# Kernel optimization log

Measured on AMD Instinct MI355X. Metric: run time of the kernel, lower is better.

The kernel has to match this reference:

```python
import jax, jax.numpy as jnp
import numpy as np

HEAD_SIZE = 64

def setup_inputs() -> dict:
    key = jax.random.key(0)
    ks = jax.random.split(key, 6)
    B, T, D, H, HS = 4, 2048, 1024, 16, HEAD_SIZE
    s = 1.0 / np.sqrt(D)
    return {
        "x": jax.random.normal(ks[0], (B, T, D), jnp.float32),
        "Wq": jax.random.normal(ks[1], (H, D, HS), jnp.float32) * s,
        "Wk": jax.random.normal(ks[2], (H, D, HS), jnp.float32) * s,
        "Wv": jax.random.normal(ks[3], (H, D, HS), jnp.float32) * s,
        "Wp": jax.random.normal(ks[4], (D, D), jnp.float32) * s,
        "bp": jnp.zeros((D,), jnp.float32),
    }

def reference(x, Wq, Wk, Wv, Wp, bp):
    B, T, D = x.shape
    H, _, HS = Wq.shape
    # per-head projections (bias-free Linears), stacked over heads
    q = jnp.einsum('btd,hde->bhte', x, Wq)
    k = jnp.einsum('btd,hde->bhte', x, Wk)
    v = jnp.einsum('btd,hde->bhte', x, Wv)
    scores = jnp.einsum('bhqe,bhke->bhqk', q, k) / jnp.sqrt(jnp.float32(HS))
    causal = jnp.tril(jnp.ones((T, T), bool))  # mask[:T,:T]
    scores = jnp.where(causal, scores, -jnp.inf)
    w = jax.nn.softmax(scores, axis=-1)  # dropout p=0.0 -> identity
    out = jnp.einsum('bhqk,bhke->bhqe', w, v)
    # concat heads along last dim: [B,T,H*HS] == [B,T,D]
    out = out.transpose(0, 2, 1, 3).reshape(B, T, H * HS)
    return out @ Wp.T + bp  # note: Wp stored as [out,in] like nn.Linear
```

## Files before the change

kernel.cpp:

```cpp
#include <hip/hip_runtime.h>
#include <hip/hip_bf16.h>

typedef unsigned short u16;
typedef unsigned int u32;
typedef __attribute__((ext_vector_type(8))) short short8;
typedef __attribute__((ext_vector_type(4))) float f32x4;

#define B_ 4
#define T_ 2048
#define D_ 1024
#define H_ 16
#define HS_ 64
#define BT (B_*T_)

__device__ __forceinline__ float bf2f(u16 b){ union{u32 u; float f;} v; v.u=((u32)b)<<16; return v.f; }
__device__ __forceinline__ u16 f2bf(float f){
    __hip_bfloat16 h = __float2bfloat16(f);
    union{__hip_bfloat16 h; u16 u;} v; v.h = h; return v.u;
}
__device__ __forceinline__ void split2(float x, u16& h, u16& l){
    u16 hb = f2bf(x);
    float fh = bf2f(hb);
    h = hb; l = f2bf(x - fh);
}
union U4 { u16 s[4]; uint2 v; };
union S8 { u16 s[8]; short8 v; };

#define GLD16(g,l) __builtin_amdgcn_global_load_lds( \
    (__attribute__((address_space(1))) void*)(u16*)(g), \
    (__attribute__((address_space(3))) void*)(l), 16, 0, 0)

__device__ __forceinline__ int swz(int row, int col){
    return row*64 + (((col>>3) ^ (row&7))<<3) + (col&7);
}
#define FCHK(r) (((r)>>1)&3)

#define DPPMV(x, ctrl) __int_as_float(__builtin_amdgcn_update_dpp(0, __float_as_int(x), (ctrl), 0xF, 0xF, true))

__global__ __launch_bounds__(256) void split_f32(const float* __restrict__ src,
                                                 u16* __restrict__ dh, u16* __restrict__ dl,
                                                 int n8)
{
    int i = blockIdx.x*256 + threadIdx.x;
    const int stride = gridDim.x*256;
    for (; i < n8; i += stride){
        float4 a = *(const float4*)(src + (size_t)i*8);
        float4 b = *(const float4*)(src + (size_t)i*8 + 4);
        S8 hh, ll;
        split2(a.x, hh.s[0], ll.s[0]); split2(a.y, hh.s[1], ll.s[1]);
        split2(a.z, hh.s[2], ll.s[2]); split2(a.w, hh.s[3], ll.s[3]);
        split2(b.x, hh.s[4], ll.s[4]); split2(b.y, hh.s[5], ll.s[5]);
        split2(b.z, hh.s[6], ll.s[6]); split2(b.w, hh.s[7], ll.s[7]);
        *(short8*)(dh + (size_t)i*8) = hh.v;
        *(short8*)(dl + (size_t)i*8) = ll.v;
    }
}

__global__ __launch_bounds__(256) void pack_w(const float* __restrict__ Wq,
                                              const float* __restrict__ Wk,
                                              const float* __restrict__ Wv,
                                              u16* __restrict__ Wth,
                                              u16* __restrict__ Wtl)
{
    __shared__ float Tl[64*68];
    const int h = blockIdx.x, dt = blockIdx.y, z = blockIdx.z;
    const float* src = (z==0) ? Wq : ((z==1) ? Wk : Wv);
    const int t = threadIdx.x;
    const int d0 = dt*64;
    #pragma unroll
    for (int i=0;i<4;++i){
        int ci = t + 256*i;
        int dr = ci>>4, ec = ci&15;
        float4 v = *(const float4*)(src + ((size_t)h*D_ + d0+dr)*HS_ + ec*4);
        *(float4*)(Tl + dr*68 + ec*4) = v;
    }
    __syncthreads();
    #pragma unroll
    for (int i=0;i<4;++i){
        int ci = t + 256*i;
        int e = ci>>4, dc = ci&15;
        U4 hh, ll;
        #pragma unroll
        for (int j=0;j<4;++j){
            float f = Tl[(dc*4+j)*68 + e];
            split2(f, hh.s[j], ll.s[j]);
        }
        int n = z*D_ + h*HS_ + e;
        *(uint2*)(Wth + (size_t)n*D_ + d0 + dc*4) = hh.v;
        *(uint2*)(Wtl + (size_t)n*D_ + d0 + dc*4) = ll.v;
    }
}

template<bool PS>
__global__ __launch_bounds__(256) void gemm_qkv(const float* __restrict__ x,
                                                const u16* __restrict__ xh, const u16* __restrict__ xl,
                                                const u16* __restrict__ Wth,
                                                const u16* __restrict__ Wtl,
                                                float* __restrict__ qo,
                                                u16* __restrict__ qho, u16* __restrict__ qlo,
                                                u16* __restrict__ kho, u16* __restrict__ klo,
                                                u16* __restrict__ vth, u16* __restrict__ vtl)
{
    __shared__ u16 Ash[128*32], Asl[128*32];
    __shared__ u16 Bsh[128*32], Bsl[128*32];
    const int n0 = blockIdx.x*128, m0 = blockIdx.y*128;
    const int t = threadIdx.x;
    const int w = t>>6, lane = t&63, quad = lane>>4, l16 = lane&15;
    const int wm = (w>>1)*64, wn = (w&1)*64;
    f32x4 acc[4][4];
    #pragma unroll
    for (int i=0;i<4;++i)
        #pragma unroll
        for (int j=0;j<4;++j) acc[i][j] = (f32x4){0.f,0.f,0.f,0.f};
    for (int kt=0; kt<32; ++kt){
        const int k0 = kt*32;
        #pragma unroll
        for (int i=0;i<2;++i){
            int ci = t + 256*i;
            int row = ci>>2, c = ci&3;
            int cs = c ^ FCHK(row);
            GLD16(Wth + (size_t)(n0+row)*D_ + k0 + cs*8, Bsh + ci*8);
            GLD16(Wtl + (size_t)(n0+row)*D_ + k0 + cs*8, Bsl + ci*8);
        }
        if constexpr(PS){
            #pragma unroll
            for (int i=0;i<2;++i){
                int ci = t + 256*i;
                int row = ci>>2, c = ci&3;
                int cs = c ^ FCHK(row);
                GLD16(xh + (size_t)(m0+row)*D_ + k0 + cs*8, Ash + ci*8);
                GLD16(xl + (size_t)(m0+row)*D_ + k0 + cs*8, Asl + ci*8);
            }
        } else {
            #pragma unroll
            for (int i=0;i<4;++i){
                int ci = t + 256*i;
                int row = ci>>3, c4 = ci&7;
                float4 av = *(const float4*)(x + (size_t)(m0+row)*D_ + k0 + c4*4);
                U4 hh, ll;
                split2(av.x, hh.s[0], ll.s[0]); split2(av.y, hh.s[1], ll.s[1]);
                split2(av.z, hh.s[2], ll.s[2]); split2(av.w, hh.s[3], ll.s[3]);
                int off = row*32 + ((((c4>>1) ^ FCHK(row))<<3) | ((c4&1)<<2));
                *(uint2*)(Ash + off) = hh.v;
                *(uint2*)(Asl + off) = ll.v;
            }
        }
        __syncthreads();
        short8 afh[4], afl[4], bfh[4], bfl[4];
        #pragma unroll
        for (int mi=0;mi<4;++mi){
            const int rr = wm+mi*16+l16;
            const int off = rr*32 + ((quad ^ FCHK(rr))<<3);
            afh[mi] = *(const short8*)(Ash + off);
            afl[mi] = *(const short8*)(Asl + off);
        }
        #pragma unroll
        for (int ni=0;ni<4;++ni){
            const int rr = wn+ni*16+l16;
            const int off = rr*32 + ((quad ^ FCHK(rr))<<3);
            bfh[ni] = *(const short8*)(Bsh + off);
            bfl[ni] = *(const short8*)(Bsl + off);
        }
        #pragma unroll
        for (int mi=0;mi<4;++mi)
            #pragma unroll
            for (int ni=0;ni<4;++ni){
                acc[mi][ni] = __builtin_amdgcn_mfma_f32_16x16x32_bf16(afh[mi], bfh[ni], acc[mi][ni], 0,0,0);
                acc[mi][ni] = __builtin_amdgcn_mfma_f32_16x16x32_bf16(afh[mi], bfl[ni], acc[mi][ni], 0,0,0);
                acc[mi][ni] = __builtin_amdgcn_mfma_f32_16x16x32_bf16(afl[mi], bfh[ni], acc[mi][ni], 0,0,0);
            }
        __syncthreads();
    }
    const int z = n0 >> 10;
    if (z <= 1){
        if constexpr(PS){
            u16* dh = z ? kho : qho;
            u16* dl = z ? klo : qlo;
            #pragma unroll
            for (int ni=0;ni<4;++ni){
                const int nloc = (n0 & 1023) + wn + ni*16 + l16;
                #pragma unroll
                for (int mi=0;mi<4;++mi){
                    const int row = m0 + wm + mi*16 + quad*4;
                    #pragma unroll
                    for (int r=0;r<4;++r){
                        u16 hh, ll; split2(acc[mi][ni][r], hh, ll);
                        dh[(size_t)(row+r)*D_ + nloc] = hh;
                        dl[(size_t)(row+r)*D_ + nloc] = ll;
                    }
                }
            }
        } else {
            if (z == 0){
                #pragma unroll
                for (int ni=0;ni<4;++ni){
                    const int nloc = (n0 & 1023) + wn + ni*16 + l16;
                    #pragma unroll
                    for (int mi=0;mi<4;++mi){
                        const int row = m0 + wm + mi*16 + quad*4;
                        #pragma unroll
                        for (int r=0;r<4;++r)
                            qo[(size_t)(row+r)*D_ + nloc] = acc[mi][ni][r];
                    }
                }
            } else {
                #pragma unroll
                for (int ni=0;ni<4;++ni){
                    const int nloc = (n0 & 1023) + wn + ni*16 + l16;
                    #pragma unroll
                    for (int mi=0;mi<4;++mi){
                        const int row = m0 + wm + mi*16 + quad*4;
                        #pragma unroll
                        for (int r=0;r<4;++r){
                            u16 hh, ll; split2(acc[mi][ni][r], hh, ll);
                            kho[(size_t)(row+r)*D_ + nloc] = hh;
                            klo[(size_t)(row+r)*D_ + nloc] = ll;
                        }
                    }
                }
            }
        }
    } else {
        #pragma unroll
        for (int ni=0;ni<4;++ni){
            const int nloc = (n0 & 1023) + wn + ni*16 + l16;
            const int hloc = nloc>>6, e = nloc&63;
            #pragma unroll
            for (int mi=0;mi<4;++mi){
                const int rowb = m0 + wm + mi*16 + quad*4;
                const int bidx = rowb >> 11, tloc = rowb & 2047;
                U4 hh, ll;
                #pragma unroll
                for (int r=0;r<4;++r) split2(acc[mi][ni][r], hh.s[r], ll.s[r]);
                const size_t adr = ((size_t)((bidx*16 + hloc)*64 + e))*T_ + tloc;
                *(uint2*)(vth + adr) = hh.v;
                *(uint2*)(vtl + adr) = ll.v;
            }
        }
    }
}

template<bool PS>
__global__ __launch_bounds__(512, 2) void attn(const float* __restrict__ qf,
                                            const u16* __restrict__ qh, const u16* __restrict__ ql,
                                            const u16* __restrict__ kh, const u16* __restrict__ kl,
                                            const u16* __restrict__ vth, const u16* __restrict__ vtl,
                                            float* __restrict__ att,
                                            u16* __restrict__ atth, u16* __restrict__ attl)
{
    __shared__ u16 Ksh[64*64], Ksl[64*64];
    __shared__ u16 Vsh[64*64], Vsl[64*64];
    __shared__ u16 Pb[8*32*64];
    const int x = blockIdx.y & 7;
    const int bh = (blockIdx.x << 3) | (blockIdx.y >> 3);
    const int b = bh >> 4, h = bh & 15;
    const int t = threadIdx.x;
    const int w = t>>6, lane = t&63, quad = lane>>4, l16 = lane&15;

    u16* Pm = Pb + w*2048;

    const int srow = t>>3, sc = t&7;
    const int slo = swz(srow, sc*8);
    uint4 pkh, pkl, pvh, pvl;
    {
        const size_t gk = ((size_t)(b*T_ + srow))*D_ + h*64 + sc*8;
        pkh = *(const uint4*)(kh + gk);
        pkl = *(const uint4*)(kl + gk);
        const size_t gv = ((size_t)(bh*64 + srow))*T_ + sc*8;
        pvh = *(const uint4*)(vth + gv);
        pvl = *(const uint4*)(vtl + gv);
    }

    #pragma unroll 1
    for (int seg=0; seg<2; ++seg){
        const int qi = seg ? x : (15 - x);
        const int qrow = qi*128 + w*16;

        short8 qh_[2], ql_[2];
        if constexpr(PS){
            const size_t qb = ((size_t)(b*T_ + qrow + l16))*D_ + h*64;
            #pragma unroll
            for (int ks=0;ks<2;++ks){
                qh_[ks] = *(const short8*)(qh + qb + ks*32 + quad*8);
                ql_[ks] = *(const short8*)(ql + qb + ks*32 + quad*8);
            }
        } else {
            const float* qp = qf + ((size_t)(b*T_ + qrow + l16))*D_ + h*64;
            #pragma unroll
            for (int ks=0;ks<2;++ks){
                float4 a0 = *(const float4*)(qp + ks*32 + quad*8);
                float4 a1 = *(const float4*)(qp + ks*32 + quad*8 + 4);
                S8 hh, ll;
                split2(a0.x, hh.s[0], ll.s[0]); split2(a0.y, hh.s[1], ll.s[1]);
                split2(a0.z, hh.s[2], ll.s[2]); split2(a0.w, hh.s[3], ll.s[3]);
                split2(a1.x, hh.s[4], ll.s[4]); split2(a1.y, hh.s[5], ll.s[5]);
                split2(a1.z, hh.s[6], ll.s[6]); split2(a1.w, hh.s[7], ll.s[7]);
                qh_[ks] = hh.v; ql_[ks] = ll.v;
            }
        }
        f32x4 o[4];
        #pragma unroll
        for (int i=0;i<4;++i) o[i] = (f32x4){0.f,0.f,0.f,0.f};
        float m_i[4], l_i[4];
        #pragma unroll
        for (int r=0;r<4;++r){ m_i[r] = -INFINITY; l_i[r] = 0.f; }

        const int kvT = 2*qi + 2;
        for (int kvt=0; kvt<kvT; ++kvt){
            __syncthreads();
            *(uint4*)(Ksh + slo) = pkh;
            *(uint4*)(Ksl + slo) = pkl;
            *(uint4*)(Vsh + slo) = pvh;
            *(uint4*)(Vsl + slo) = pvl;
            __syncthreads();

            const int nk = (kvt+1 < kvT) ? (kvt+1) : ((seg==0) ? 0 : -1);
            if (nk >= 0){
                const size_t gk = ((size_t)(b*T_ + nk*64 + srow))*D_ + h*64 + sc*8;
                pkh = *(const uint4*)(kh + gk);
                pkl = *(const uint4*)(kl + gk);
                const size_t gv = ((size_t)(bh*64 + srow))*T_ + nk*64 + sc*8;
                pvh = *(const uint4*)(vth + gv);
                pvl = *(const uint4*)(vtl + gv);
            }

            float s[4][4];
            __builtin_amdgcn_s_setprio(1);
            #pragma unroll
            for (int ni=0;ni<4;++ni){
                f32x4 sa = (f32x4){0.f,0.f,0.f,0.f};
                const int row = ni*16 + l16;
                #pragma unroll
                for (int ks=0;ks<2;++ks){
                    const int co = swz(row, ks*32 + quad*8);
                    short8 k8h = *(const short8*)(Ksh + co);
                    short8 k8l = *(const short8*)(Ksl + co);
                    sa = __builtin_amdgcn_mfma_f32_16x16x32_bf16(qh_[ks], k8h, sa, 0,0,0);
                    sa = __builtin_amdgcn_mfma_f32_16x16x32_bf16(qh_[ks], k8l, sa, 0,0,0);
                    sa = __builtin_amdgcn_mfma_f32_16x16x32_bf16(ql_[ks], k8h, sa, 0,0,0);
                }
                #pragma unroll
                for (int r=0;r<4;++r) s[ni][r] = sa[r]*0.125f;
            }
            __builtin_amdgcn_s_setprio(0);
            if (kvt*64 + 63 > qrow){
                #pragma unroll
                for (int ni=0;ni<4;++ni){
                    const int colabs = kvt*64 + ni*16 + l16;
                    #pragma unroll
                    for (int r=0;r<4;++r){
                        const int rowabs = qrow + quad*4 + r;
                        if (colabs > rowabs) s[ni][r] = -INFINITY;
                    }
                }
            }
            float alpha[4];
            #pragma unroll
            for (int r=0;r<4;++r){
                float rm = fmaxf(fmaxf(s[0][r],s[1][r]), fmaxf(s[2][r],s[3][r]));
                rm = fmaxf(rm, DPPMV(rm, 0xB1));
                rm = fmaxf(rm, DPPMV(rm, 0x4E));
                rm = fmaxf(rm, DPPMV(rm, 0x124));
                rm = fmaxf(rm, DPPMV(rm, 0x128));
                const float mnew = fmaxf(m_i[r], rm);
                alpha[r] = __expf(m_i[r] - mnew);
                m_i[r] = mnew;
                #pragma unroll
                for (int ni=0;ni<4;++ni) s[ni][r] = __expf(s[ni][r] - mnew);
                float rs = s[0][r]+s[1][r]+s[2][r]+s[3][r];
                rs += DPPMV(rs, 0xB1);
                rs += DPPMV(rs, 0x4E);
                rs += DPPMV(rs, 0x124);
                rs += DPPMV(rs, 0x128);
                l_i[r] = l_i[r]*alpha[r] + rs;
            }
            #pragma unroll
            for (int ni=0;ni<4;++ni)
                #pragma unroll
                for (int r=0;r<4;++r) o[ni][r] *= alpha[r];

            u16 ph[4][4], pl[4][4];
            #pragma unroll
            for (int ni=0;ni<4;++ni)
                #pragma unroll
                for (int r=0;r<4;++r)
                    split2(s[ni][r], ph[ni][r], pl[ni][r]);
            #pragma unroll
            for (int ni=0;ni<4;++ni)
                #pragma unroll
                for (int r=0;r<4;++r){
                    Pm[swz(quad*4+r,      ni*16 + l16)] = ph[ni][r];
                    Pm[swz(16 + quad*4+r, ni*16 + l16)] = pl[ni][r];
                }
            __asm__ volatile("s_waitcnt lgkmcnt(0)" ::: "memory");
            short8 pah[2], pal[2];
            #pragma unroll
            for (int ks=0;ks<2;++ks){
                pah[ks] = *(const short8*)(Pm + swz(l16,      ks*32 + quad*8));
                pal[ks] = *(const short8*)(Pm + swz(16 + l16, ks*32 + quad*8));
            }

            __builtin_amdgcn_s_setprio(1);
            #pragma unroll
            for (int ni=0;ni<4;++ni){
                const int row = ni*16 + l16;
                #pragma unroll
                for (int ks=0;ks<2;++ks){
                    const int co = swz(row, ks*32 + quad*8);
                    short8 v8h = *(const short8*)(Vsh + co);
                    short8 v8l = *(const short8*)(Vsl + co);
                    o[ni] = __builtin_amdgcn_mfma_f32_16x16x32_bf16(pah[ks], v8h, o[ni], 0,0,0);
                    o[ni] = __builtin_amdgcn_mfma_f32_16x16x32_bf16(pah[ks], v8l, o[ni], 0,0,0);
                    o[ni] = __builtin_amdgcn_mfma_f32_16x16x32_bf16(pal[ks], v8h, o[ni], 0,0,0);
                }
            }
            __builtin_amdgcn_s_setprio(0);
        }
        const size_t ob = (size_t)(b*T_ + qrow);
        #pragma unroll
        for (int ni=0;ni<4;++ni){
            const int col = h*64 + ni*16 + l16;
            #pragma unroll
            for (int r=0;r<4;++r){
                const float v = o[ni][r] / l_i[r];
                const size_t idx = (ob + quad*4 + r)*D_ + col;
                if constexpr(PS){
                    u16 hh, ll; split2(v, hh, ll);
                    atth[idx] = hh; attl[idx] = ll;
                } else {
                    att[idx] = v;
                }
            }
        }
    }
}

template<bool PS>
__global__ __launch_bounds__(256) void gemm_bt(const float* __restrict__ A,
                                               const u16* __restrict__ Ath, const u16* __restrict__ Atl,
                                               const float* __restrict__ Bt,
                                               const u16* __restrict__ Bth, const u16* __restrict__ Btl,
                                               float* __restrict__ C,
                                               const float* __restrict__ bias,
                                               int M, int N, int K)
{
    __shared__ u16 Ash[128*32], Asl[128*32];
    __shared__ u16 Bsh[128*32], Bsl[128*32];
    const int n0 = blockIdx.x*128, m0 = blockIdx.y*128;
    const int t = threadIdx.x;
    const int w = t>>6, lane = t&63, quad = lane>>4, l16 = lane&15;
    const int wm = (w>>1)*64, wn = (w&1)*64;
    f32x4 acc[4][4];
    #pragma unroll
    for (int i=0;i<4;++i)
        #pragma unroll
        for (int j=0;j<4;++j) acc[i][j] = (f32x4){0.f,0.f,0.f,0.f};
    const int kT = K >> 5;
    for (int kt=0; kt<kT; ++kt){
        const int k0 = kt*32;
        if constexpr(PS){
            #pragma unroll
            for (int i=0;i<2;++i){
                int ci = t + 256*i;
                int row = ci>>2, c = ci&3;
                int cs = c ^ FCHK(row);
                GLD16(Ath + (size_t)(m0+row)*K + k0 + cs*8, Ash + ci*8);
                GLD16(Atl + (size_t)(m0+row)*K + k0 + cs*8, Asl + ci*8);
                GLD16(Bth + (size_t)(n0+row)*K + k0 + cs*8, Bsh + ci*8);
                GLD16(Btl + (size_t)(n0+row)*K + k0 + cs*8, Bsl + ci*8);
            }
        } else {
            #pragma unroll
            for (int i=0;i<4;++i){
                int ci = t + 256*i;
                int row = ci>>3, c4 = ci&7;
                float4 av = *(const float4*)(A  + (size_t)(m0+row)*K + k0 + c4*4);
                float4 bv = *(const float4*)(Bt + (size_t)(n0+row)*K + k0 + c4*4);
                U4 ah, al, bh, bl;
                split2(av.x, ah.s[0], al.s[0]); split2(av.y, ah.s[1], al.s[1]);
                split2(av.z, ah.s[2], al.s[2]); split2(av.w, ah.s[3], al.s[3]);
                split2(bv.x, bh.s[0], bl.s[0]); split2(bv.y, bh.s[1], bl.s[1]);
                split2(bv.z, bh.s[2], bl.s[2]); split2(bv.w, bh.s[3], bl.s[3]);
                int off = row*32 + ((((c4>>1) ^ FCHK(row))<<3) | ((c4&1)<<2));
                *(uint2*)(Ash + off) = ah.v;
                *(uint2*)(Asl + off) = al.v;
                *(uint2*)(Bsh + off) = bh.v;
                *(uint2*)(Bsl + off) = bl.v;
            }
        }
        __syncthreads();
        short8 afh[4], afl[4], bfh[4], bfl[4];
        #pragma unroll
        for (int mi=0;mi<4;++mi){
            const int rr = wm+mi*16+l16;
            const int off = rr*32 + ((quad ^ FCHK(rr))<<3);
            afh[mi] = *(const short8*)(Ash + off);
            afl[mi] = *(const short8*)(Asl + off);
        }
        #pragma unroll
        for (int ni=0;ni<4;++ni){
            const int rr = wn+ni*16+l16;
            const int off = rr*32 + ((quad ^ FCHK(rr))<<3);
            bfh[ni] = *(const short8*)(Bsh + off);
            bfl[ni] = *(const short8*)(Bsl + off);
        }
        #pragma unroll
        for (int mi=0;mi<4;++mi)
            #pragma unroll
            for (int ni=0;ni<4;++ni){
                acc[mi][ni] = __builtin_amdgcn_mfma_f32_16x16x32_bf16(afh[mi], bfh[ni], acc[mi][ni], 0,0,0);
                acc[mi][ni] = __builtin_amdgcn_mfma_f32_16x16x32_bf16(afh[mi], bfl[ni], acc[mi][ni], 0,0,0);
                acc[mi][ni] = __builtin_amdgcn_mfma_f32_16x16x32_bf16(afl[mi], bfh[ni], acc[mi][ni], 0,0,0);
            }
        __syncthreads();
    }
    #pragma unroll
    for (int ni=0;ni<4;++ni){
        const int col = n0 + wn + ni*16 + l16;
        const float bv = bias ? bias[col] : 0.f;
        #pragma unroll
        for (int mi=0;mi<4;++mi){
            const int row = m0 + wm + mi*16 + quad*4;
            #pragma unroll
            for (int r=0;r<4;++r)
                C[(size_t)(row+r)*N + col] = acc[mi][ni][r] + bv;
        }
    }
}

extern "C" void kernel_launch(void* const* d_in, const int* in_sizes, int n_in,
                              void* d_out, int out_size, void* d_ws, size_t ws_size,
                              hipStream_t stream)
{
    const float* x  = (const float*)d_in[0];
    const float* Wq = (const float*)d_in[1];
    const float* Wk = (const float*)d_in[2];
    const float* Wv = (const float*)d_in[3];
    const float* Wp = (const float*)d_in[4];
    const float* bp = (const float*)d_in[5];
    float* out = (float*)d_out;

    const size_t NE = (size_t)BT*D_;
    const size_t NEED = (10*NE + 2*(size_t)D_*D_)*2;

    if (ws_size >= NEED){
        u16* xh   = (u16*)d_ws;
        u16* xl   = xh + NE;
        u16* qh   = xl + NE;
        u16* ql   = qh + NE;
        u16* kh   = ql + NE;
        u16* kl   = kh + NE;
        u16* vth  = kl + NE;
        u16* vtl  = vth + NE;
        u16* atth = vtl + NE;
        u16* attl = atth + NE;
        u16* Wph  = attl + NE;
        u16* Wpl  = Wph + (size_t)D_*D_;
        u16* Wth  = atth;
        u16* Wtl  = Wth + (size_t)3072*D_;

        split_f32<<<1024, 256, 0, stream>>>(x,  xh,  xl,  (int)(NE/8));
        split_f32<<<512,  256, 0, stream>>>(Wp, Wph, Wpl, (int)(((size_t)D_*D_)/8));
        pack_w   <<<dim3(16,16,3), 256, 0, stream>>>(Wq, Wk, Wv, Wth, Wtl);
        gemm_qkv<true><<<dim3(24, BT/128), 256, 0, stream>>>(x, xh, xl, Wth, Wtl,
                                                             nullptr, qh, ql, kh, kl, vth, vtl);
        attn<true><<<dim3(T_/256, B_*H_), 512, 0, stream>>>(nullptr, qh, ql, kh, kl, vth, vtl,
                                                            nullptr, atth, attl);
        gemm_bt<true><<<dim3(8, BT/128), 256, 0, stream>>>(nullptr, atth, attl,
                                                           nullptr, Wph, Wpl,
                                                           out, bp, BT, D_, D_);
    } else {
        float* q   = (float*)d_ws;
        u16*  kh   = (u16*)(q + NE);
        u16*  kl   = kh + NE;
        u16*  vth  = kl + NE;
        u16*  vtl  = vth + NE;
        float* att = (float*)(vtl + NE);
        u16*  Wth  = (u16*)att;
        u16*  Wtl  = Wth + (size_t)3072*D_;

        pack_w   <<<dim3(16,16,3), 256, 0, stream>>>(Wq, Wk, Wv, Wth, Wtl);
        gemm_qkv<false><<<dim3(24, BT/128), 256, 0, stream>>>(x, nullptr, nullptr, Wth, Wtl,
                                                              q, nullptr, nullptr, kh, kl, vth, vtl);
        attn<false><<<dim3(T_/256, B_*H_), 512, 0, stream>>>(q, nullptr, nullptr, kh, kl, vth, vtl,
                                                             att, nullptr, nullptr);
        gemm_bt<false><<<dim3(8, BT/128), 256, 0, stream>>>(att, nullptr, nullptr,
                                                            Wp, nullptr, nullptr,
                                                            out, bp, BT, D_, D_);
    }
}
```

Baseline: 492.7 us.

## Shrink attention blocks to 4 waves with 64-row query tiles and halved P buffer

The attention kernel now runs 256-thread blocks, four waves covering 64 query rows, instead of 512-thread blocks covering 128 rows. The grid is remapped to 8x128 with paired causal tiles (31-px, px), and each thread loads two 16-byte chunks per K/V tile. The per-wave P staging buffer is halved by writing the high and low bf16 halves in sequence through the same space. The second barrier now comes after issuing the next tile's global loads. The aim is higher occupancy and finer load balance, at the cost of more K/V reloads per query row and an extra LDS round trip for P.

Result: slower. 659.3 us (+33.8%).

```diff
diff --git a/kernel.cpp b/kernel.cpp
--- a/kernel.cpp
+++ b/kernel.cpp
@@ -241,7 +241,7 @@
 }
 
 template<bool PS>
-__global__ __launch_bounds__(512, 2) void attn(const float* __restrict__ qf,
+__global__ __launch_bounds__(256, 4) void attn(const float* __restrict__ qf,
                                             const u16* __restrict__ qh, const u16* __restrict__ ql,
                                             const u16* __restrict__ kh, const u16* __restrict__ kl,
                                             const u16* __restrict__ vth, const u16* __restrict__ vtl,
@@ -250,31 +250,33 @@
 {
     __shared__ u16 Ksh[64*64], Ksl[64*64];
     __shared__ u16 Vsh[64*64], Vsl[64*64];
-    __shared__ u16 Pb[8*32*64];
-    const int x = blockIdx.y & 7;
-    const int bh = (blockIdx.x << 3) | (blockIdx.y >> 3);
+    __shared__ u16 Pb[4*16*64];
+    const int bx = blockIdx.x, by = blockIdx.y;
+    const int bh = ((by & 7) << 3) | bx;
+    const int px = by >> 3;
     const int b = bh >> 4, h = bh & 15;
     const int t = threadIdx.x;
     const int w = t>>6, lane = t&63, quad = lane>>4, l16 = lane&15;
 
-    u16* Pm = Pb + w*2048;
-
-    const int srow = t>>3, sc = t&7;
-    const int slo = swz(srow, sc*8);
-    uint4 pkh, pkl, pvh, pvl;
+    u16* Pm = Pb + w*1024;
+
+    const int srow = t>>2, sc = t&3;
+    const int slo0 = swz(srow, sc*8);
+    const int slo1 = swz(srow, sc*8 + 32);
+    uint4 pkh0, pkh1, pkl0, pkl1, pvh0, pvh1, pvl0, pvl1;
     {
         const size_t gk = ((size_t)(b*T_ + srow))*D_ + h*64 + sc*8;
-        pkh = *(const uint4*)(kh + gk);
-        pkl = *(const uint4*)(kl + gk);
+        pkh0 = *(const uint4*)(kh + gk);  pkh1 = *(const uint4*)(kh + gk + 32);
+        pkl0 = *(const uint4*)(kl + gk);  pkl1 = *(const uint4*)(kl + gk + 32);
         const size_t gv = ((size_t)(bh*64 + srow))*T_ + sc*8;
-        pvh = *(const uint4*)(vth + gv);
-        pvl = *(const uint4*)(vtl + gv);
+        pvh0 = *(const uint4*)(vth + gv); pvh1 = *(const uint4*)(vth + gv + 32);
+        pvl0 = *(const uint4*)(vtl + gv); pvl1 = *(const uint4*)(vtl + gv + 32);
     }
 
     #pragma unroll 1
     for (int seg=0; seg<2; ++seg){
-        const int qi = seg ? x : (15 - x);
-        const int qrow = qi*128 + w*16;
+        const int qi = seg ? px : (31 - px);
+        const int qrow = qi*64 + w*16;
 
         short8 qh_[2], ql_[2];
         if constexpr(PS){
@@ -305,24 +307,23 @@
         #pragma unroll
         for (int r=0;r<4;++r){ m_i[r] = -INFINITY; l_i[r] = 0.f; }
 
-        const int kvT = 2*qi + 2;
+        const int kvT = qi + 1;
         for (int kvt=0; kvt<kvT; ++kvt){
             __syncthreads();
-            *(uint4*)(Ksh + slo) = pkh;
-            *(uint4*)(Ksl + slo) = pkl;
-            *(uint4*)(Vsh + slo) = pvh;
-            *(uint4*)(Vsl + slo) = pvl;
-            __syncthreads();
-
+            *(uint4*)(Ksh + slo0) = pkh0;  *(uint4*)(Ksh + slo1) = pkh1;
+            *(uint4*)(Ksl + slo0) = pkl0;  *(uint4*)(Ksl + slo1) = pkl1;
+            *(uint4*)(Vsh + slo0) = pvh0;  *(uint4*)(Vsh + slo1) = pvh1;
+            *(uint4*)(Vsl + slo0) = pvl0;  *(uint4*)(Vsl + slo1) = pvl1;
             const int nk = (kvt+1 < kvT) ? (kvt+1) : ((seg==0) ? 0 : -1);
             if (nk >= 0){
                 const size_t gk = ((size_t)(b*T_ + nk*64 + srow))*D_ + h*64 + sc*8;
-                pkh = *(const uint4*)(kh + gk);
-                pkl = *(const uint4*)(kl + gk);
+                pkh0 = *(const uint4*)(kh + gk);  pkh1 = *(const uint4*)(kh + gk + 32);
+                pkl0 = *(const uint4*)(kl + gk);  pkl1 = *(const uint4*)(kl + gk + 32);
                 const size_t gv = ((size_t)(bh*64 + srow))*T_ + nk*64 + sc*8;
-                pvh = *(const uint4*)(vth + gv);
-                pvl = *(const uint4*)(vtl + gv);
-            }
+                pvh0 = *(const uint4*)(vth + gv); pvh1 = *(const uint4*)(vth + gv + 32);
+                pvl0 = *(const uint4*)(vtl + gv); pvl1 = *(const uint4*)(vtl + gv + 32);
+            }
+            __syncthreads();
 
             float s[4][4];
             __builtin_amdgcn_s_setprio(1);
@@ -388,17 +389,24 @@
             #pragma unroll
             for (int ni=0;ni<4;++ni)
                 #pragma unroll
-                for (int r=0;r<4;++r){
-                    Pm[swz(quad*4+r,      ni*16 + l16)] = ph[ni][r];
-                    Pm[swz(16 + quad*4+r, ni*16 + l16)] = pl[ni][r];
-                }
+                for (int r=0;r<4;++r)
+                    Pm[swz(quad*4+r, ni*16 + l16)] = ph[ni][r];
             __asm__ volatile("s_waitcnt lgkmcnt(0)" ::: "memory");
             short8 pah[2], pal[2];
             #pragma unroll
-            for (int ks=0;ks<2;++ks){
-                pah[ks] = *(const short8*)(Pm + swz(l16,      ks*32 + quad*8));
-                pal[ks] = *(const short8*)(Pm + swz(16 + l16, ks*32 + quad*8));
-            }
+            for (int ks=0;ks<2;++ks)
+                pah[ks] = *(const short8*)(Pm + swz(l16, ks*32 + quad*8));
+            __asm__ volatile("" ::: "memory");
+            #pragma unroll
+            for (int ni=0;ni<4;++ni)
+                #pragma unroll
+                for (int r=0;r<4;++r)
+                    Pm[swz(quad*4+r, ni*16 + l16)] = pl[ni][r];
+            __asm__ volatile("s_waitcnt lgkmcnt(0)" ::: "memory");
+            #pragma unroll
+            for (int ks=0;ks<2;++ks)
+                pal[ks] = *(const short8*)(Pm + swz(l16, ks*32 + quad*8));
+            __asm__ volatile("" ::: "memory");
 
             __builtin_amdgcn_s_setprio(1);
             #pragma unroll
@@ -564,8 +572,8 @@
         pack_w   <<<dim3(16,16,3), 256, 0, stream>>>(Wq, Wk, Wv, Wth, Wtl);
         gemm_qkv<true><<<dim3(24, BT/128), 256, 0, stream>>>(x, xh, xl, Wth, Wtl,
                                                              nullptr, qh, ql, kh, kl, vth, vtl);
-        attn<true><<<dim3(T_/256, B_*H_), 512, 0, stream>>>(nullptr, qh, ql, kh, kl, vth, vtl,
-                                                            nullptr, atth, attl);
+        attn<true><<<dim3(8, 128), 256, 0, stream>>>(nullptr, qh, ql, kh, kl, vth, vtl,
+                                                     nullptr, atth, attl);
         gemm_bt<true><<<dim3(8, BT/128), 256, 0, stream>>>(nullptr, atth, attl,
                                                            nullptr, Wph, Wpl,
                                                            out, bp, BT, D_, D_);
@@ -582,8 +590,8 @@
         pack_w   <<<dim3(16,16,3), 256, 0, stream>>>(Wq, Wk, Wv, Wth, Wtl);
         gemm_qkv<false><<<dim3(24, BT/128), 256, 0, stream>>>(x, nullptr, nullptr, Wth, Wtl,
                                                               q, nullptr, nullptr, kh, kl, vth, vtl);
-        attn<false><<<dim3(T_/256, B_*H_), 512, 0, stream>>>(q, nullptr, nullptr, kh, kl, vth, vtl,
-                                                             att, nullptr, nullptr);
+        attn<false><<<dim3(8, 128), 256, 0, stream>>>(q, nullptr, nullptr, kh, kl, vth, vtl,
+                                                      att, nullptr, nullptr);
         gemm_bt<false><<<dim3(8, BT/128), 256, 0, stream>>>(att, nullptr, nullptr,
                                                             Wp, nullptr, nullptr,
                                                             out, bp, BT, D_, D_);
```
